# Kernel optimization log

Hardware: AMD Instinct MI355X
Metric: run time of the kernel (lower is better)

## Reference

```python
import jax, jax.numpy as jnp
import numpy as np

N = 8192
E = 262144
C = 256          # in_channels
OUT = 256        # out_channels
H = 4            # num_heads
DH = C // H      # head dim


def setup_inputs() -> dict:
    key = jax.random.key(0)
    ks = jax.random.split(key, 12)
    stdv = 1.0 / np.sqrt(C)
    inp = {
        "x": jax.random.normal(ks[0], (N, C), dtype=jnp.float32),
        "adj": jax.random.randint(ks[1], (2, E), 0, N, dtype=jnp.int64),
        "weight_local": jax.random.uniform(ks[2], (C, C), jnp.float32, -stdv, stdv),
        # nn.MultiheadAttention packed projections
        "in_proj_w": jax.random.normal(ks[3], (3 * C, C), jnp.float32) * stdv,
        "in_proj_b": jnp.zeros((3 * C,), jnp.float32),
        "out_proj_w": jax.random.normal(ks[4], (C, C), jnp.float32) * stdv,
        "out_proj_b": jnp.zeros((C,), jnp.float32),
        "ln_g": jnp.ones((C,), jnp.float32),
        "ln_b": jnp.zeros((C,), jnp.float32),
        "alpha": jnp.zeros((), jnp.float32),
        "fc_w": jax.random.normal(ks[5], (OUT, C), jnp.float32) * stdv,
        "fc_b": jnp.zeros((OUT,), jnp.float32),
    }
    return inp


def _gcn_conv(x, edge_index):
    # out[col] += (1/sqrt(d[col]*d[row])) * x[row], d = in-degree by col
    row, col = edge_index[0], edge_index[1]
    n = x.shape[0]
    d = jax.ops.segment_sum(jnp.ones((edge_index.shape[1],), x.dtype), col, num_segments=n)
    val = jax.lax.rsqrt(d[col] * d[row])
    val = jnp.where(jnp.isfinite(val), val, 0.0)
    msg = x[row] * val[:, None]                      # [E, C] gather + scale
    return jax.ops.segment_sum(msg, col, num_segments=n)  # [N, C] scatter-add


def _mha(x, in_proj_w, in_proj_b, out_proj_w, out_proj_b):
    # single-batch self-attention over all N nodes
    qkv = x @ in_proj_w.T + in_proj_b                # [N, 3C]
    q, k, v = jnp.split(qkv, 3, axis=-1)
    def heads(t):
        return t.reshape(N, H, DH).transpose(1, 0, 2)  # [H, N, DH]
    q, k, v = heads(q), heads(k), heads(v)
    scores = jnp.einsum("hnd,hmd->hnm", q, k) / np.sqrt(DH)  # [H, N, N]
    attn = jax.nn.softmax(scores, axis=-1)
    out = jnp.einsum("hnm,hmd->hnd", attn, v)        # [H, N, DH]
    out = out.transpose(1, 0, 2).reshape(N, C)
    return out @ out_proj_w.T + out_proj_b


def _layernorm(x, g, b, eps=1e-5):
    mu = jnp.mean(x, axis=-1, keepdims=True)
    var = jnp.var(x, axis=-1, keepdims=True)
    return (x - mu) * jax.lax.rsqrt(var + eps) * g + b


def reference(x, adj, weight_local, in_proj_w, in_proj_b, out_proj_w, out_proj_b,
              ln_g, ln_b, alpha, fc_w, fc_b):
    hi = _gcn_conv(x, adj)
    local_embed = hi @ weight_local                   # [N, C]
    attn_out = _mha(x, in_proj_w, in_proj_b, out_proj_w, out_proj_b)
    global_embed = _layernorm(x + attn_out, ln_g, ln_b)
    w = jax.nn.sigmoid(alpha)
    combined = w * local_embed + (1.0 - w) * global_embed
    return combined @ fc_w.T + fc_b                   # [N, OUT]
```

## Files before the change

### kernel.cpp

```cpp
#include <hip/hip_runtime.h>
#include <hip/hip_bf16.h>
#include <math.h>

#define NN   8192
#define EE   262144
#define CC   256
#define HH   4

typedef __bf16 bf16;
typedef __bf16 bf16x8 __attribute__((ext_vector_type(8)));
typedef __bf16 bf16x4 __attribute__((ext_vector_type(4)));
typedef __bf16 bf16x2 __attribute__((ext_vector_type(2)));
typedef float  f32x4  __attribute__((ext_vector_type(4)));

static __device__ __forceinline__ bf16 f2bf(float f) { return (bf16)f; }

static __device__ __forceinline__ unsigned pk2(float a, float b) {
    __hip_bfloat162 h = __float22bfloat162_rn(float2{a, b});
    return *reinterpret_cast<unsigned*>(&h);
}

__global__ void prep_all(const float* __restrict__ x, bf16* __restrict__ xb,
                         const float* __restrict__ ipw, const float* __restrict__ opw,
                         const float* __restrict__ fcw, const float* __restrict__ wloc,
                         bf16* __restrict__ ipwb, bf16* __restrict__ opwb,
                         bf16* __restrict__ fcwb, bf16* __restrict__ wlTb,
                         const int* __restrict__ adj, int* __restrict__ ideg) {
    int b = blockIdx.x, t = threadIdx.x;
    if (b < 2048) {
        for (int i = b * 256 + t; i < NN * CC; i += 2048 * 256) xb[i] = f2bf(x[i]);
    } else if (b < 2816) { int i = (b - 2048) * 256 + t; ipwb[i] = f2bf(ipw[i]); }
    else if (b < 3072)   { int i = (b - 2816) * 256 + t; opwb[i] = f2bf(opw[i]); }
    else if (b < 3328)   { int i = (b - 3072) * 256 + t; fcwb[i] = f2bf(fcw[i]); }
    else if (b < 3584)   { int n = b - 3328;             wlTb[n * 256 + t] = f2bf(wloc[t * 256 + n]); }
    else {
        int e = (b - 3584) * 256 + t;
        if (e < EE) atomicAdd(&ideg[adj[EE + e]], 1);
    }
}

__global__ __launch_bounds__(256) void build_kv(const bf16* __restrict__ qkv,
                                                bf16* __restrict__ Kpk,
                                                bf16* __restrict__ Vpk) {
    __shared__ bf16 tl[64][72];
    const int bx = blockIdx.x;
    const int h  = blockIdx.y;
    const int tid = threadIdx.x;
    #pragma unroll
    for (int i = 0; i < 2; i++) {
        int u = tid + i * 256;
        int key = u >> 3, g = u & 7;
        *reinterpret_cast<bf16x8*>(&tl[key][g * 8]) =
            *reinterpret_cast<const bf16x8*>(qkv + (size_t)(bx * 64 + key) * 768 + 256 + h * 64 + g * 8);
    }
    __syncthreads();
    #pragma unroll
    for (int i = 0; i < 2; i++) {
        int ee = tid + i * 256;
        int l15 = ee & 15, quad = (ee >> 4) & 3, c = (ee >> 6) & 1, ktl = ee >> 7;
        int key_local = (ktl >> 1) * 32 + (l15 >> 2) * 8 + (ktl & 1) * 4 + (l15 & 3);
        bf16x8 v = *reinterpret_cast<const bf16x8*>(&tl[key_local][c * 32 + quad * 8]);
        *reinterpret_cast<bf16x8*>(Kpk + ((size_t)((h * 512 + bx * 4 + ktl) * 2 + c)) * 512
                                       + (quad * 16 + l15) * 8) = v;
    }
    __syncthreads();
    #pragma unroll
    for (int i = 0; i < 2; i++) {
        int u = tid + i * 256;
        int key = u >> 3, g = u & 7;
        *reinterpret_cast<bf16x8*>(&tl[key][g * 8]) =
            *reinterpret_cast<const bf16x8*>(qkv + (size_t)(bx * 64 + key) * 768 + 512 + h * 64 + g * 8);
    }
    __syncthreads();
    #pragma unroll
    for (int i = 0; i < 2; i++) {
        int ee = tid + i * 256;
        int l15 = ee & 15, quad = (ee >> 4) & 3, nt = (ee >> 6) & 3, kcl = ee >> 8;
        bf16x8 v;
        #pragma unroll
        for (int j = 0; j < 8; j++) v[j] = tl[kcl * 32 + quad * 8 + j][nt * 16 + l15];
        *reinterpret_cast<bf16x8*>(Vpk + ((size_t)((h * 256 + bx * 2 + kcl) * 4 + nt)) * 512
                                       + (quad * 16 + l15) * 8) = v;
    }
}

__global__ __launch_bounds__(256) void scan_offsets(const int* __restrict__ ideg,
        int* __restrict__ off, int* __restrict__ cursor, float* __restrict__ rs) {
    __shared__ int ps[256];
    const int tid = threadIdx.x;
    const int base = tid * 32;
    int loc[32];
    int s = 0;
    #pragma unroll
    for (int i = 0; i < 32; i++) { loc[i] = s; s += ideg[base + i]; }
    ps[tid] = s;
    __syncthreads();
    for (int d = 1; d < 256; d <<= 1) {
        int v = (tid >= d) ? ps[tid - d] : 0;
        __syncthreads();
        ps[tid] += v;
        __syncthreads();
    }
    int excl = ps[tid] - s;
    #pragma unroll
    for (int i = 0; i < 32; i++) {
        int o = excl + loc[i];
        off[base + i] = o;
        cursor[base + i] = o;
        int dg = ideg[base + i];
        rs[base + i] = dg > 0 ? rsqrtf((float)dg) : 0.f;
    }
    if (tid == 255) off[8192] = excl + s;
}

__global__ void fill_csr(const int* __restrict__ adj, int* __restrict__ cursor,
                         int* __restrict__ csr) {
    int e = blockIdx.x * 256 + threadIdx.x;
    if (e < EE) {
        int col = adj[EE + e];
        int pos = atomicAdd(&cursor[col], 1);
        csr[pos] = adj[e];
    }
}

__global__ __launch_bounds__(256) void gcn_gather3(const bf16* __restrict__ xb,
        const int* __restrict__ csr, const int* __restrict__ off,
        const float* __restrict__ rs, bf16* __restrict__ hib) {
    const int node = blockIdx.x * 2 + (threadIdx.x >> 7);
    const int j = threadIdx.x & 127;
    const int o = off[node];
    const int cnt = off[node + 1] - o;
    const float rsc = rs[node];
    const unsigned* xrow = (const unsigned*)xb;
    float a0 = 0.f, a1 = 0.f;
    int e = 0;
    for (; e + 8 <= cnt; e += 8) {
        int r[8];
        float v[8];
        unsigned u[8];
        #pragma unroll
        for (int i = 0; i < 8; i++) r[i] = csr[o + e + i];
        #pragma unroll
        for (int i = 0; i < 8; i++) v[i] = rsc * rs[r[i]];
        #pragma unroll
        for (int i = 0; i < 8; i++) u[i] = xrow[(size_t)r[i] * 128 + j];
        #pragma unroll
        for (int i = 0; i < 8; i++) {
            a0 += __uint_as_float(u[i] << 16) * v[i];
            a1 += __uint_as_float(u[i] & 0xffff0000u) * v[i];
        }
    }
    for (; e < cnt; e++) {
        int r0 = csr[o + e];
        float v0 = rsc * rs[r0];
        unsigned u0 = xrow[(size_t)r0 * 128 + j];
        a0 += __uint_as_float(u0 << 16) * v0;
        a1 += __uint_as_float(u0 & 0xffff0000u) * v0;
    }
    bf16x2 pk;
    pk[0] = f2bf(a0);
    pk[1] = f2bf(a1);
    ((bf16x2*)(hib + (size_t)node * CC))[j] = pk;
}

__global__ __launch_bounds__(256) void gemm_bt(
        const bf16* __restrict__ A, const bf16* __restrict__ W,
        const float* __restrict__ bias,
        float* __restrict__ outF, bf16* __restrict__ outB,
        int M, int N, int K) {
    const int tid  = threadIdx.x;
    const int wave = tid >> 6;
    const int lane = tid & 63;
    const int quad = lane >> 4;
    const int l15  = lane & 15;
    const int m0 = blockIdx.x * 128;
    const int n0 = blockIdx.y * 64;

    __shared__ bf16 Alds[128][72];
    __shared__ bf16 Wlds[64][72];

    f32x4 acc[2][4];
    #pragma unroll
    for (int mt = 0; mt < 2; mt++)
        #pragma unroll
        for (int nt = 0; nt < 4; nt++)
            acc[mt][nt] = (f32x4){0.f, 0.f, 0.f, 0.f};

    for (int k0 = 0; k0 < K; k0 += 64) {
        #pragma unroll
        for (int i = 0; i < 4; i++) {
            int u = tid + i * 256;
            int r = u >> 3;
            int cp = u & 7;
            *reinterpret_cast<bf16x8*>(&Alds[r][cp * 8]) =
                *reinterpret_cast<const bf16x8*>(A + (size_t)(m0 + r) * K + k0 + cp * 8);
        }
        #pragma unroll
        for (int i = 0; i < 2; i++) {
            int u = tid + i * 256;
            int r = u >> 3;
            int cp = u & 7;
            *reinterpret_cast<bf16x8*>(&Wlds[r][cp * 8]) =
                *reinterpret_cast<const bf16x8*>(W + (size_t)(n0 + r) * K + k0 + cp * 8);
        }
        __syncthreads();
        #pragma unroll
        for (int c = 0; c < 2; c++) {
            bf16x8 af[2], wf[4];
            #pragma unroll
            for (int mt = 0; mt < 2; mt++)
                af[mt] = *reinterpret_cast<const bf16x8*>(&Alds[wave * 32 + mt * 16 + l15][c * 32 + quad * 8]);
            #pragma unroll
            for (int nt = 0; nt < 4; nt++)
                wf[nt] = *reinterpret_cast<const bf16x8*>(&Wlds[nt * 16 + l15][c * 32 + quad * 8]);
            #pragma unroll
            for (int mt = 0; mt < 2; mt++)
                #pragma unroll
                for (int nt = 0; nt < 4; nt++)
                    acc[mt][nt] = __builtin_amdgcn_mfma_f32_16x16x32_bf16(af[mt], wf[nt], acc[mt][nt], 0, 0, 0);
        }
        __syncthreads();
    }
    #pragma unroll
    for (int mt = 0; mt < 2; mt++)
        #pragma unroll
        for (int nt = 0; nt < 4; nt++)
            #pragma unroll
            for (int r = 0; r < 4; r++) {
                int m = m0 + wave * 32 + mt * 16 + quad * 4 + r;
                int n = n0 + nt * 16 + l15;
                float v = acc[mt][nt][r];
                if (bias) v += bias[n];
                if (outF) outF[(size_t)m * N + n] = v;
                else      outB[(size_t)m * N + n] = f2bf(v);
            }
}

__global__ __launch_bounds__(512, 2) void flash_attn10(const bf16* __restrict__ qkv,
                                                       const bf16* __restrict__ Kpk,
                                                       const bf16* __restrict__ Vpk,
                                                       bf16* __restrict__ attnO) {
    const int tid  = threadIdx.x;
    const int w    = tid >> 6;
    const int g    = w >> 2;
    const int k4   = w & 3;
    const int lane = tid & 63;
    const int quad = lane >> 4;
    const int l15  = lane & 15;
    const int bx = blockIdx.x;
    const int h  = bx & 3;
    const int qb = bx >> 2;
    const int qbase = qb * 128 + g * 64;

    __shared__ bf16 Osh[8][64][68];
    __shared__ float lsh[8][64];

    const float qs = 0.180336880f;
    bf16x8 qf[4][2];
    #pragma unroll
    for (int qt = 0; qt < 4; qt++)
        #pragma unroll
        for (int c = 0; c < 2; c++) {
            bf16x8 raw = *reinterpret_cast<const bf16x8*>(
                qkv + (size_t)(qbase + qt * 16 + l15) * 768 + h * 64 + c * 32 + quad * 8);
            #pragma unroll
            for (int j = 0; j < 8; j++) qf[qt][c][j] = f2bf((float)raw[j] * qs);
        }

    const bf16* Kb = Kpk + (size_t)h * 524288 + lane * 8;
    const bf16* Vb = Vpk + (size_t)h * 524288 + lane * 8;

    f32x4 oacc[4][4];
    #pragma unroll
    for (int qt = 0; qt < 4; qt++)
        #pragma unroll
        for (int nt = 0; nt < 4; nt++) oacc[qt][nt] = (f32x4){0.f, 0.f, 0.f, 0.f};
    f32x4 lacc[4];
    #pragma unroll
    for (int qt = 0; qt < 4; qt++) lacc[qt] = (f32x4){0.f, 0.f, 0.f, 0.f};
    bf16x8 onesf;
    #pragma unroll
    for (int j = 0; j < 8; j++) onesf[j] = f2bf(1.0f);
    const f32x4 z4 = (f32x4){0.f, 0.f, 0.f, 0.f};

    bf16x8 kfA[2][2], vfA[4], kfB[2][2], vfB[4];

    #define LOADKV(kc, kf, vf)                                                          \
        {                                                                               \
            _Pragma("unroll")                                                           \
            for (int s = 0; s < 2; s++)                                                 \
                _Pragma("unroll")                                                       \
                for (int c = 0; c < 2; c++)                                             \
                    kf[s][c] = *reinterpret_cast<const bf16x8*>(Kb + (kc) * 2048 + s * 1024 + c * 512); \
            _Pragma("unroll")                                                           \
            for (int nt = 0; nt < 4; nt++)                                              \
                vf[nt] = *reinterpret_cast<const bf16x8*>(Vb + (kc) * 2048 + nt * 512); \
        }

    #define COMPUTE(kf, vf)                                                             \
        {                                                                               \
            f32x4 sacc[2][4];                                                           \
            _Pragma("unroll")                                                           \
            for (int s = 0; s < 2; s++)                                                 \
                _Pragma("unroll")                                                       \
                for (int qt = 0; qt < 4; qt++) {                                        \
                    sacc[s][qt] = __builtin_amdgcn_mfma_f32_16x16x32_bf16(kf[s][0], qf[qt][0], z4, 0, 0, 0); \
                    sacc[s][qt] = __builtin_amdgcn_mfma_f32_16x16x32_bf16(kf[s][1], qf[qt][1], sacc[s][qt], 0, 0, 0); \
                }                                                                       \
            _Pragma("unroll")                                                           \
            for (int qt = 0; qt < 4; qt++) {                                            \
                float e0 = __builtin_amdgcn_exp2f(sacc[0][qt][0]);                      \
                float e1 = __builtin_amdgcn_exp2f(sacc[0][qt][1]);                      \
                float e2 = __builtin_amdgcn_exp2f(sacc[0][qt][2]);                      \
                float e3 = __builtin_amdgcn_exp2f(sacc[0][qt][3]);                      \
                float e4 = __builtin_amdgcn_exp2f(sacc[1][qt][0]);                      \
                float e5 = __builtin_amdgcn_exp2f(sacc[1][qt][1]);                      \
                float e6 = __builtin_amdgcn_exp2f(sacc[1][qt][2]);                      \
                float e7 = __builtin_amdgcn_exp2f(sacc[1][qt][3]);                      \
                union { bf16x8 v; unsigned u[4]; } pu;                                  \
                pu.u[0] = pk2(e0, e1);                                                  \
                pu.u[1] = pk2(e2, e3);                                                  \
                pu.u[2] = pk2(e4, e5);                                                  \
                pu.u[3] = pk2(e6, e7);                                                  \
                _Pragma("unroll")                                                       \
                for (int nt = 0; nt < 4; nt++)                                          \
                    oacc[qt][nt] = __builtin_amdgcn_mfma_f32_16x16x32_bf16(pu.v, vf[nt], oacc[qt][nt], 0, 0, 0); \
                lacc[qt] = __builtin_amdgcn_mfma_f32_16x16x32_bf16(pu.v, onesf, lacc[qt], 0, 0, 0); \
            }                                                                           \
        }

    LOADKV(k4, kfA, vfA);
    for (int it = 0; it < 64; it += 2) {
        const int kB = k4 + (it + 1) * 4;
        LOADKV(kB, kfB, vfB);
        COMPUTE(kfA, vfA);
        int kA2 = k4 + (it + 2) * 4;
        if (kA2 > 255) kA2 = k4;
        LOADKV(kA2, kfA, vfA);
        COMPUTE(kfB, vfB);
    }
    #undef LOADKV
    #undef COMPUTE

    #pragma unroll
    for (int qt = 0; qt < 4; qt++)
        #pragma unroll
        for (int nt = 0; nt < 4; nt++)
            #pragma unroll
            for (int r = 0; r < 4; r++)
                Osh[w][qt * 16 + quad * 4 + r][nt * 16 + l15] = f2bf(oacc[qt][nt][r]);
    if (l15 == 0) {
        #pragma unroll
        for (int qt = 0; qt < 4; qt++)
            #pragma unroll
            for (int r = 0; r < 4; r++)
                lsh[w][qt * 16 + quad * 4 + r] = lacc[qt][r];
    }
    __syncthreads();

    const int q7 = tid >> 2;
    const int gg = q7 >> 6;
    const int ql = q7 & 63;
    const int ds = (tid & 3) * 16;
    const int wb = gg * 4;
    float lsum = lsh[wb][ql] + lsh[wb + 1][ql] + lsh[wb + 2][ql] + lsh[wb + 3][ql];
    float linv = 1.f / lsum;
    float acc[16];
    #pragma unroll
    for (int i = 0; i < 16; i++) acc[i] = 0.f;
    #pragma unroll
    for (int v = 0; v < 4; v++) {
        bf16x8 o0 = *reinterpret_cast<const bf16x8*>(&Osh[wb + v][ql][ds]);
        bf16x8 o1 = *reinterpret_cast<const bf16x8*>(&Osh[wb + v][ql][ds + 8]);
        #pragma unroll
        for (int i = 0; i < 8; i++) { acc[i] += (float)o0[i]; acc[8 + i] += (float)o1[i]; }
    }
    bf16x8 ob0, ob1;
    #pragma unroll
    for (int i = 0; i < 8; i++) {
        ob0[i] = f2bf(acc[i] * linv);
        ob1[i] = f2bf(acc[8 + i] * linv);
    }
    bf16* dst = attnO + (size_t)(qb * 128 + q7) * CC + h * 64 + ds;
    *reinterpret_cast<bf16x8*>(dst) = ob0;
    *reinterpret_cast<bf16x8*>(dst + 8) = ob1;
}

__global__ __launch_bounds__(256) void gemm_ln_fc(
        const bf16* __restrict__ aOb, const bf16* __restrict__ opwb, const float* __restrict__ opb,
        const bf16* __restrict__ hib, const bf16* __restrict__ wlTb,
        const float* __restrict__ x, const float* __restrict__ lng, const float* __restrict__ lnb,
        const float* __restrict__ alp, const bf16* __restrict__ fcwb, const float* __restrict__ fcb,
        float* __restrict__ out) {
    const int tid = threadIdx.x;
    const int w = tid >> 6, lane = tid & 63, quad = lane >> 4, l15 = lane & 15;
    const int m0 = blockIdx.x * 16;
    const int n0w = w * 64;
    const f32x4 z4 = (f32x4){0.f, 0.f, 0.f, 0.f};

    __shared__ bf16 Ab[16][264];
    __shared__ float Xl[16][260];
    __shared__ float rsum[4][16], rsq[4][16];

    #pragma unroll
    for (int i = 0; i < 4; i++) {
        int u = tid + i * 256;
        int row = u >> 6, cp = (u & 63) * 4;
        *reinterpret_cast<f32x4*>(&Xl[row][cp]) =
            *reinterpret_cast<const f32x4*>(x + (size_t)(m0 + row) * CC + cp);
    }

    #pragma unroll
    for (int i = 0; i < 2; i++) {
        int u = tid + i * 256;
        int row = u >> 5, cp = (u & 31) * 8;
        *reinterpret_cast<bf16x8*>(&Ab[row][cp]) =
            *reinterpret_cast<const bf16x8*>(aOb + (size_t)(m0 + row) * CC + cp);
    }
    __syncthreads();
    f32x4 r0[4], r1[4], acc[4];
    #pragma unroll
    for (int nt = 0; nt < 4; nt++) acc[nt] = z4;
    for (int kc = 0; kc < 4; kc++)
        #pragma unroll
        for (int c = 0; c < 2; c++) {
            bf16x8 af = *reinterpret_cast<const bf16x8*>(&Ab[l15][kc * 64 + c * 32 + quad * 8]);
            #pragma unroll
            for (int nt = 0; nt < 4; nt++) {
                bf16x8 wf = *reinterpret_cast<const bf16x8*>(
                    opwb + (size_t)(n0w + nt * 16 + l15) * CC + kc * 64 + c * 32 + quad * 8);
                acc[nt] = __builtin_amdgcn_mfma_f32_16x16x32_bf16(af, wf, acc[nt], 0, 0, 0);
            }
        }
    #pragma unroll
    for (int nt = 0; nt < 4; nt++) r0[nt] = acc[nt];
    __syncthreads();

    #pragma unroll
    for (int i = 0; i < 2; i++) {
        int u = tid + i * 256;
        int row = u >> 5, cp = (u & 31) * 8;
        *reinterpret_cast<bf16x8*>(&Ab[row][cp]) =
            *reinterpret_cast<const bf16x8*>(hib + (size_t)(m0 + row) * CC + cp);
    }
    __syncthreads();
    #pragma unroll
    for (int nt = 0; nt < 4; nt++) acc[nt] = z4;
    for (int kc = 0; kc < 4; kc++)
        #pragma unroll
        for (int c = 0; c < 2; c++) {
            bf16x8 af = *reinterpret_cast<const bf16x8*>(&Ab[l15][kc * 64 + c * 32 + quad * 8]);
            #pragma unroll
            for (int nt = 0; nt < 4; nt++) {
                bf16x8 wf = *reinterpret_cast<const bf16x8*>(
                    wlTb + (size_t)(n0w + nt * 16 + l15) * CC + kc * 64 + c * 32 + quad * 8);
                acc[nt] = __builtin_amdgcn_mfma_f32_16x16x32_bf16(af, wf, acc[nt], 0, 0, 0);
            }
        }
    #pragma unroll
    for (int nt = 0; nt < 4; nt++) r1[nt] = acc[nt];
    __syncthreads();

    float v[4][4];
    #pragma unroll
    for (int nt = 0; nt < 4; nt++) {
        float bias0 = opb[n0w + nt * 16 + l15];
        #pragma unroll
        for (int r = 0; r < 4; r++)
            v[nt][r] = Xl[quad * 4 + r][n0w + nt * 16 + l15] + r0[nt][r] + bias0;
    }
    #pragma unroll
    for (int r = 0; r < 4; r++) {
        float s = v[0][r] + v[1][r] + v[2][r] + v[3][r];
        float s2 = v[0][r] * v[0][r] + v[1][r] * v[1][r] + v[2][r] * v[2][r] + v[3][r] * v[3][r];
        #pragma unroll
        for (int o = 1; o < 16; o <<= 1) { s += __shfl_xor(s, o); s2 += __shfl_xor(s2, o); }
        if (l15 == 0) { rsum[w][quad * 4 + r] = s; rsq[w][quad * 4 + r] = s2; }
    }
    __syncthreads();

    const float wgt = 1.f / (1.f + __expf(-alp[0]));
    float gv[4], bv[4], fb[4];
    #pragma unroll
    for (int nt = 0; nt < 4; nt++) {
        int n = n0w + nt * 16 + l15;
        gv[nt] = lng[n]; bv[nt] = lnb[n]; fb[nt] = fcb[n];
    }
    #pragma unroll
    for (int r = 0; r < 4; r++) {
        int row = quad * 4 + r;
        float S = rsum[0][row] + rsum[1][row] + rsum[2][row] + rsum[3][row];
        float S2 = rsq[0][row] + rsq[1][row] + rsq[2][row] + rsq[3][row];
        float mu = S * (1.f / CC);
        float var = S2 * (1.f / CC) - mu * mu;
        float rstd = rsqrtf(var + 1e-5f);
        #pragma unroll
        for (int nt = 0; nt < 4; nt++) {
            float ln = (v[nt][r] - mu) * rstd * gv[nt] + bv[nt];
            float cmb = wgt * r1[nt][r] + (1.f - wgt) * ln;
            Ab[row][n0w + nt * 16 + l15] = f2bf(cmb);
        }
    }
    __syncthreads();

    #pragma unroll
    for (int nt = 0; nt < 4; nt++) acc[nt] = z4;
    for (int kc = 0; kc < 4; kc++)
        #pragma unroll
        for (int c = 0; c < 2; c++) {
            bf16x8 af = *reinterpret_cast<const bf16x8*>(&Ab[l15][kc * 64 + c * 32 + quad * 8]);
            #pragma unroll
            for (int nt = 0; nt < 4; nt++) {
                bf16x8 wf = *reinterpret_cast<const bf16x8*>(
                    fcwb + (size_t)(n0w + nt * 16 + l15) * CC + kc * 64 + c * 32 + quad * 8);
                acc[nt] = __builtin_amdgcn_mfma_f32_16x16x32_bf16(af, wf, acc[nt], 0, 0, 0);
            }
        }
    #pragma unroll
    for (int nt = 0; nt < 4; nt++)
        #pragma unroll
        for (int r = 0; r < 4; r++)
            out[(size_t)(m0 + quad * 4 + r) * CC + n0w + nt * 16 + l15] = acc[nt][r] + fb[nt];
}

extern "C" void kernel_launch(void* const* d_in, const int* in_sizes, int n_in,
                              void* d_out, int out_size, void* d_ws, size_t ws_size,
                              hipStream_t stream) {
    (void)in_sizes; (void)n_in; (void)out_size; (void)ws_size;
    const float* x    = (const float*)d_in[0];
    const int*   adj  = (const int*)d_in[1];
    const float* wloc = (const float*)d_in[2];
    const float* ipw  = (const float*)d_in[3];
    const float* ipb  = (const float*)d_in[4];
    const float* opw  = (const float*)d_in[5];
    const float* opb  = (const float*)d_in[6];
    const float* lng  = (const float*)d_in[7];
    const float* lnb  = (const float*)d_in[8];
    const float* alp  = (const float*)d_in[9];
    const float* fcw  = (const float*)d_in[10];
    const float* fcb  = (const float*)d_in[11];
    float* out = (float*)d_out;

    char* p = (char*)d_ws;
    int*   ideg   = (int*)p;    p += (size_t)NN * 4;
    int*   off    = (int*)p;    p += (size_t)(NN + 1) * 4;
    int*   cursor = (int*)p;    p += (size_t)NN * 4;
    float* rs     = (float*)p;  p += (size_t)NN * 4;
    int*   csr    = (int*)p;    p += (size_t)EE * 4;
    bf16* xb    = (bf16*)p;   p += (size_t)NN * CC * 2;
    bf16* hib   = (bf16*)p;   p += (size_t)NN * CC * 2;
    bf16* ipwb  = (bf16*)p;   p += (size_t)768 * 256 * 2;
    bf16* wlTb  = (bf16*)p;   p += (size_t)256 * 256 * 2;
    bf16* opwb  = (bf16*)p;   p += (size_t)256 * 256 * 2;
    bf16* fcwb  = (bf16*)p;   p += (size_t)256 * 256 * 2;
    bf16* qkvb  = (bf16*)p;   p += (size_t)NN * 768 * 2;
    bf16* Kpk   = (bf16*)p;   p += (size_t)HH * 512 * 2 * 512 * 2;
    bf16* Vpk   = (bf16*)p;   p += (size_t)HH * 256 * 4 * 512 * 2;
    bf16* aOb   = (bf16*)p;   p += (size_t)NN * CC * 2;

    hipMemsetAsync(ideg, 0, (size_t)NN * 4, stream);

    prep_all<<<4608, 256, 0, stream>>>(x, xb, ipw, opw, fcw, wloc, ipwb, opwb, fcwb, wlTb, adj, ideg);
    scan_offsets<<<1, 256, 0, stream>>>(ideg, off, cursor, rs);
    fill_csr<<<EE / 256, 256, 0, stream>>>(adj, cursor, csr);
    gcn_gather3<<<NN / 2, 256, 0, stream>>>(xb, csr, off, rs, hib);

    gemm_bt<<<dim3(NN / 128, 768 / 64), 256, 0, stream>>>(xb, ipwb, ipb, nullptr, qkvb, NN, 768, 256);
    build_kv<<<dim3(NN / 64, HH), 256, 0, stream>>>(qkvb, Kpk, Vpk);
    flash_attn10<<<256, 512, 0, stream>>>(qkvb, Kpk, Vpk, aOb);
    gemm_ln_fc<<<NN / 16, 256, 0, stream>>>(aOb, opwb, opb, hib, wlTb, x, lng, lnb, alp, fcwb, fcb, out);
}
```

Measured before the change: 249.4 us.

## Stage shared K/V tiles in LDS via async global-to-LDS loads in flash attention

The attention kernel now has both 4-wave groups of a block share one K/V tile. That tile is double-buffered in shared memory and filled with global_load_lds, replacing per-wave direct register loads from global memory. The query tile per wave group drops from 64 to 32 rows, so the grid doubles to 512 blocks and the occupancy hint rises to 4. The O/l reduction buffers reuse the K/V shared memory. This aims to halve global K/V traffic per block and improve latency hiding, at the cost of a block-wide barrier every iteration and fewer queries reusing each loaded K/V fragment.

```diff
diff --git a/kernel.cpp b/kernel.cpp
--- a/kernel.cpp
+++ b/kernel.cpp
@@ -18,6 +18,11 @@
 static __device__ __forceinline__ unsigned pk2(float a, float b) {
     __hip_bfloat162 h = __float22bfloat162_rn(float2{a, b});
     return *reinterpret_cast<unsigned*>(&h);
+}
+
+static __device__ __forceinline__ void gload_lds16(const bf16* g, bf16* l) {
+    __builtin_amdgcn_global_load_lds((const __attribute__((address_space(1))) void*)g,
+                                     (__attribute__((address_space(3))) void*)l, 16, 0, 0);
 }
 
 __global__ void prep_all(const float* __restrict__ x, bf16* __restrict__ xb,
@@ -236,7 +241,7 @@
             }
 }
 
-__global__ __launch_bounds__(512, 2) void flash_attn10(const bf16* __restrict__ qkv,
+__global__ __launch_bounds__(512, 4) void flash_attn11(const bf16* __restrict__ qkv,
                                                        const bf16* __restrict__ Kpk,
                                                        const bf16* __restrict__ Vpk,
                                                        bf16* __restrict__ attnO) {
@@ -250,65 +255,69 @@
     const int bx = blockIdx.x;
     const int h  = bx & 3;
     const int qb = bx >> 2;
-    const int qbase = qb * 128 + g * 64;
-
-    __shared__ bf16 Osh[8][64][68];
-    __shared__ float lsh[8][64];
+    const int qbase = qb * 64;
+
+    __shared__ bf16 KV[2][16384];
 
     const float qs = 0.180336880f;
-    bf16x8 qf[4][2];
-    #pragma unroll
-    for (int qt = 0; qt < 4; qt++)
+    bf16x8 qf[2][2];
+    #pragma unroll
+    for (int qt = 0; qt < 2; qt++)
         #pragma unroll
         for (int c = 0; c < 2; c++) {
             bf16x8 raw = *reinterpret_cast<const bf16x8*>(
-                qkv + (size_t)(qbase + qt * 16 + l15) * 768 + h * 64 + c * 32 + quad * 8);
+                qkv + (size_t)(qbase + g * 32 + qt * 16 + l15) * 768 + h * 64 + c * 32 + quad * 8);
             #pragma unroll
             for (int j = 0; j < 8; j++) qf[qt][c][j] = f2bf((float)raw[j] * qs);
         }
 
-    const bf16* Kb = Kpk + (size_t)h * 524288 + lane * 8;
-    const bf16* Vb = Vpk + (size_t)h * 524288 + lane * 8;
-
-    f32x4 oacc[4][4];
-    #pragma unroll
-    for (int qt = 0; qt < 4; qt++)
+    f32x4 oacc[2][4];
+    #pragma unroll
+    for (int qt = 0; qt < 2; qt++)
         #pragma unroll
         for (int nt = 0; nt < 4; nt++) oacc[qt][nt] = (f32x4){0.f, 0.f, 0.f, 0.f};
-    f32x4 lacc[4];
-    #pragma unroll
-    for (int qt = 0; qt < 4; qt++) lacc[qt] = (f32x4){0.f, 0.f, 0.f, 0.f};
+    f32x4 lacc[2];
+    #pragma unroll
+    for (int qt = 0; qt < 2; qt++) lacc[qt] = (f32x4){0.f, 0.f, 0.f, 0.f};
     bf16x8 onesf;
     #pragma unroll
     for (int j = 0; j < 8; j++) onesf[j] = f2bf(1.0f);
     const f32x4 z4 = (f32x4){0.f, 0.f, 0.f, 0.f};
 
-    bf16x8 kfA[2][2], vfA[4], kfB[2][2], vfB[4];
-
-    #define LOADKV(kc, kf, vf)                                                          \
+    const bf16* ssrc = (g == 0 ? Kpk : Vpk) + (size_t)h * 524288 + (size_t)lane * 8;
+    const int dbase = (g ? 8192 : 0) + k4 * 2048;
+
+    #define STAGE(buf, step)                                                            \
         {                                                                               \
+            size_t sb = (size_t)((step) * 4 + k4) * 2048;                               \
+            _Pragma("unroll")                                                           \
+            for (int i = 0; i < 4; i++)                                                 \
+                gload_lds16(ssrc + sb + i * 512, &KV[buf][dbase + i * 512]);            \
+        }
+
+    #define COMPUTE(buf)                                                                \
+        {                                                                               \
+            bf16x8 kf[2][2], vf[4];                                                     \
             _Pragma("unroll")                                                           \
             for (int s = 0; s < 2; s++)                                                 \
                 _Pragma("unroll")                                                       \
                 for (int c = 0; c < 2; c++)                                             \
-                    kf[s][c] = *reinterpret_cast<const bf16x8*>(Kb + (kc) * 2048 + s * 1024 + c * 512); \
+                    kf[s][c] = *reinterpret_cast<const bf16x8*>(                        \
+                        &KV[buf][k4 * 2048 + s * 1024 + c * 512 + lane * 8]);           \
             _Pragma("unroll")                                                           \
             for (int nt = 0; nt < 4; nt++)                                              \
-                vf[nt] = *reinterpret_cast<const bf16x8*>(Vb + (kc) * 2048 + nt * 512); \
-        }
-
-    #define COMPUTE(kf, vf)                                                             \
-        {                                                                               \
-            f32x4 sacc[2][4];                                                           \
+                vf[nt] = *reinterpret_cast<const bf16x8*>(                              \
+                    &KV[buf][8192 + k4 * 2048 + nt * 512 + lane * 8]);                  \
+            f32x4 sacc[2][2];                                                           \
             _Pragma("unroll")                                                           \
             for (int s = 0; s < 2; s++)                                                 \
                 _Pragma("unroll")                                                       \
-                for (int qt = 0; qt < 4; qt++) {                                        \
+                for (int qt = 0; qt < 2; qt++) {                                        \
                     sacc[s][qt] = __builtin_amdgcn_mfma_f32_16x16x32_bf16(kf[s][0], qf[qt][0], z4, 0, 0, 0); \
                     sacc[s][qt] = __builtin_amdgcn_mfma_f32_16x16x32_bf16(kf[s][1], qf[qt][1], sacc[s][qt], 0, 0, 0); \
                 }                                                                       \
             _Pragma("unroll")                                                           \
-            for (int qt = 0; qt < 4; qt++) {                                            \
+            for (int qt = 0; qt < 2; qt++) {                                            \
                 float e0 = __builtin_amdgcn_exp2f(sacc[0][qt][0]);                      \
                 float e1 = __builtin_amdgcn_exp2f(sacc[0][qt][1]);                      \
                 float e2 = __builtin_amdgcn_exp2f(sacc[0][qt][2]);                      \
@@ -329,21 +338,22 @@
             }                                                                           \
         }
 
-    LOADKV(k4, kfA, vfA);
-    for (int it = 0; it < 64; it += 2) {
-        const int kB = k4 + (it + 1) * 4;
-        LOADKV(kB, kfB, vfB);
-        COMPUTE(kfA, vfA);
-        int kA2 = k4 + (it + 2) * 4;
-        if (kA2 > 255) kA2 = k4;
-        LOADKV(kA2, kfA, vfA);
-        COMPUTE(kfB, vfB);
-    }
-    #undef LOADKV
+    STAGE(0, 0);
+    __syncthreads();
+    for (int it = 0; it < 64; ++it) {
+        const int cur = it & 1;
+        if (it < 63) STAGE(cur ^ 1, it + 1);
+        COMPUTE(cur);
+        __syncthreads();
+    }
+    #undef STAGE
     #undef COMPUTE
 
-    #pragma unroll
-    for (int qt = 0; qt < 4; qt++)
+    bf16 (*Osh)[32][68] = reinterpret_cast<bf16 (*)[32][68]>(&KV[0][0]);
+    float* lshp = reinterpret_cast<float*>(reinterpret_cast<char*>(&KV[0][0]) + 34816);
+
+    #pragma unroll
+    for (int qt = 0; qt < 2; qt++)
         #pragma unroll
         for (int nt = 0; nt < 4; nt++)
             #pragma unroll
@@ -351,39 +361,34 @@
                 Osh[w][qt * 16 + quad * 4 + r][nt * 16 + l15] = f2bf(oacc[qt][nt][r]);
     if (l15 == 0) {
         #pragma unroll
-        for (int qt = 0; qt < 4; qt++)
+        for (int qt = 0; qt < 2; qt++)
             #pragma unroll
             for (int r = 0; r < 4; r++)
-                lsh[w][qt * 16 + quad * 4 + r] = lacc[qt][r];
-    }
-    __syncthreads();
-
-    const int q7 = tid >> 2;
-    const int gg = q7 >> 6;
-    const int ql = q7 & 63;
-    const int ds = (tid & 3) * 16;
-    const int wb = gg * 4;
-    float lsum = lsh[wb][ql] + lsh[wb + 1][ql] + lsh[wb + 2][ql] + lsh[wb + 3][ql];
+                lshp[w * 32 + qt * 16 + quad * 4 + r] = lacc[qt][r];
+    }
+    __syncthreads();
+
+    const int q6 = tid >> 3;
+    const int ds = (tid & 7) * 8;
+    const int gq = q6 >> 5;
+    const int ql = q6 & 31;
+    const int wb = gq * 4;
+    float lsum = lshp[wb * 32 + ql] + lshp[(wb + 1) * 32 + ql]
+               + lshp[(wb + 2) * 32 + ql] + lshp[(wb + 3) * 32 + ql];
     float linv = 1.f / lsum;
-    float acc[16];
-    #pragma unroll
-    for (int i = 0; i < 16; i++) acc[i] = 0.f;
+    float acc[8];
+    #pragma unroll
+    for (int i = 0; i < 8; i++) acc[i] = 0.f;
     #pragma unroll
     for (int v = 0; v < 4; v++) {
-        bf16x8 o0 = *reinterpret_cast<const bf16x8*>(&Osh[wb + v][ql][ds]);
-        bf16x8 o1 = *reinterpret_cast<const bf16x8*>(&Osh[wb + v][ql][ds + 8]);
-        #pragma unroll
-        for (int i = 0; i < 8; i++) { acc[i] += (float)o0[i]; acc[8 + i] += (float)o1[i]; }
-    }
-    bf16x8 ob0, ob1;
-    #pragma unroll
-    for (int i = 0; i < 8; i++) {
-        ob0[i] = f2bf(acc[i] * linv);
-        ob1[i] = f2bf(acc[8 + i] * linv);
-    }
-    bf16* dst = attnO + (size_t)(qb * 128 + q7) * CC + h * 64 + ds;
-    *reinterpret_cast<bf16x8*>(dst) = ob0;
-    *reinterpret_cast<bf16x8*>(dst + 8) = ob1;
+        bf16x8 o = *reinterpret_cast<const bf16x8*>(&Osh[wb + v][ql][ds]);
+        #pragma unroll
+        for (int i = 0; i < 8; i++) acc[i] += (float)o[i];
+    }
+    bf16x8 ob;
+    #pragma unroll
+    for (int i = 0; i < 8; i++) ob[i] = f2bf(acc[i] * linv);
+    *reinterpret_cast<bf16x8*>(attnO + (size_t)(qbase + q6) * CC + h * 64 + ds) = ob;
 }
 
 __global__ __launch_bounds__(256) void gemm_ln_fc(
@@ -567,6 +572,6 @@
 
     gemm_bt<<<dim3(NN / 128, 768 / 64), 256, 0, stream>>>(xb, ipwb, ipb, nullptr, qkvb, NN, 768, 256);
     build_kv<<<dim3(NN / 64, HH), 256, 0, stream>>>(qkvb, Kpk, Vpk);
-    flash_attn10<<<256, 512, 0, stream>>>(qkvb, Kpk, Vpk, aOb);
+    flash_attn11<<<512, 512, 0, stream>>>(qkvb, Kpk, Vpk, aOb);
     gemm_ln_fc<<<NN / 16, 256, 0, stream>>>(aOb, opwb, opb, hib, wlTb, x, lng, lnb, alp, fcwb, fcb, out);
 }
```

New measurement: 267.6 us. +7.3%, slower.

## Split attention keys across two blocks and combine partial sums in a new kernel

Applied to the files above, without the earlier changes.

Splits the flash-attention key range in half, so 512 blocks each process half the keys. Each block writes unnormalized fp32 partial outputs and row sums, and a new combine kernel adds the two halves and normalizes. The goal is to fill more CUs, since 256 blocks underfilled the GPU. The change also raises the launch-bounds occupancy hint and adds s_setprio around the MFMA sections. In exchange it pays for an extra kernel launch and the round trip of the fp32 partials through memory.

```diff
diff --git a/kernel.cpp b/kernel.cpp
--- a/kernel.cpp
+++ b/kernel.cpp
@@ -236,10 +236,11 @@
             }
 }
 
-__global__ __launch_bounds__(512, 2) void flash_attn10(const bf16* __restrict__ qkv,
+__global__ __launch_bounds__(512, 4) void flash_attn14(const bf16* __restrict__ qkv,
                                                        const bf16* __restrict__ Kpk,
                                                        const bf16* __restrict__ Vpk,
-                                                       bf16* __restrict__ attnO) {
+                                                       float* __restrict__ Opf,
+                                                       float* __restrict__ lpf) {
     const int tid  = threadIdx.x;
     const int w    = tid >> 6;
     const int g    = w >> 2;
@@ -249,8 +250,10 @@
     const int l15  = lane & 15;
     const int bx = blockIdx.x;
     const int h  = bx & 3;
-    const int qb = bx >> 2;
+    const int qb = (bx >> 2) & 63;
+    const int kh = bx >> 8;
     const int qbase = qb * 128 + g * 64;
+    const int cb = kh * 128;
 
     __shared__ bf16 Osh[8][64][68];
     __shared__ float lsh[8][64];
@@ -291,15 +294,16 @@
             for (int s = 0; s < 2; s++)                                                 \
                 _Pragma("unroll")                                                       \
                 for (int c = 0; c < 2; c++)                                             \
-                    kf[s][c] = *reinterpret_cast<const bf16x8*>(Kb + (kc) * 2048 + s * 1024 + c * 512); \
+                    kf[s][c] = *reinterpret_cast<const bf16x8*>(Kb + (size_t)(kc) * 2048 + s * 1024 + c * 512); \
             _Pragma("unroll")                                                           \
             for (int nt = 0; nt < 4; nt++)                                              \
-                vf[nt] = *reinterpret_cast<const bf16x8*>(Vb + (kc) * 2048 + nt * 512); \
+                vf[nt] = *reinterpret_cast<const bf16x8*>(Vb + (size_t)(kc) * 2048 + nt * 512); \
         }
 
     #define COMPUTE(kf, vf)                                                             \
         {                                                                               \
             f32x4 sacc[2][4];                                                           \
+            __builtin_amdgcn_s_setprio(1);                                              \
             _Pragma("unroll")                                                           \
             for (int s = 0; s < 2; s++)                                                 \
                 _Pragma("unroll")                                                       \
@@ -307,6 +311,7 @@
                     sacc[s][qt] = __builtin_amdgcn_mfma_f32_16x16x32_bf16(kf[s][0], qf[qt][0], z4, 0, 0, 0); \
                     sacc[s][qt] = __builtin_amdgcn_mfma_f32_16x16x32_bf16(kf[s][1], qf[qt][1], sacc[s][qt], 0, 0, 0); \
                 }                                                                       \
+            __builtin_amdgcn_s_setprio(0);                                              \
             _Pragma("unroll")                                                           \
             for (int qt = 0; qt < 4; qt++) {                                            \
                 float e0 = __builtin_amdgcn_exp2f(sacc[0][qt][0]);                      \
@@ -322,20 +327,22 @@
                 pu.u[1] = pk2(e2, e3);                                                  \
                 pu.u[2] = pk2(e4, e5);                                                  \
                 pu.u[3] = pk2(e6, e7);                                                  \
+                __builtin_amdgcn_s_setprio(1);                                          \
                 _Pragma("unroll")                                                       \
                 for (int nt = 0; nt < 4; nt++)                                          \
                     oacc[qt][nt] = __builtin_amdgcn_mfma_f32_16x16x32_bf16(pu.v, vf[nt], oacc[qt][nt], 0, 0, 0); \
                 lacc[qt] = __builtin_amdgcn_mfma_f32_16x16x32_bf16(pu.v, onesf, lacc[qt], 0, 0, 0); \
+                __builtin_amdgcn_s_setprio(0);                                          \
             }                                                                           \
         }
 
-    LOADKV(k4, kfA, vfA);
-    for (int it = 0; it < 64; it += 2) {
-        const int kB = k4 + (it + 1) * 4;
+    LOADKV(cb + k4, kfA, vfA);
+    for (int it = 0; it < 32; it += 2) {
+        const int kB = cb + k4 + (it + 1) * 4;
         LOADKV(kB, kfB, vfB);
         COMPUTE(kfA, vfA);
-        int kA2 = k4 + (it + 2) * 4;
-        if (kA2 > 255) kA2 = k4;
+        int kA2 = cb + k4 + (it + 2) * 4;
+        if (it + 2 >= 32) kA2 = cb + k4;
         LOADKV(kA2, kfA, vfA);
         COMPUTE(kfB, vfB);
     }
@@ -364,7 +371,6 @@
     const int ds = (tid & 3) * 16;
     const int wb = gg * 4;
     float lsum = lsh[wb][ql] + lsh[wb + 1][ql] + lsh[wb + 2][ql] + lsh[wb + 3][ql];
-    float linv = 1.f / lsum;
     float acc[16];
     #pragma unroll
     for (int i = 0; i < 16; i++) acc[i] = 0.f;
@@ -375,15 +381,35 @@
         #pragma unroll
         for (int i = 0; i < 8; i++) { acc[i] += (float)o0[i]; acc[8 + i] += (float)o1[i]; }
     }
-    bf16x8 ob0, ob1;
-    #pragma unroll
-    for (int i = 0; i < 8; i++) {
-        ob0[i] = f2bf(acc[i] * linv);
-        ob1[i] = f2bf(acc[8 + i] * linv);
-    }
-    bf16* dst = attnO + (size_t)(qb * 128 + q7) * CC + h * 64 + ds;
-    *reinterpret_cast<bf16x8*>(dst) = ob0;
-    *reinterpret_cast<bf16x8*>(dst + 8) = ob1;
+    float* od = Opf + (size_t)bx * 8192 + q7 * 64 + ds;
+    #pragma unroll
+    for (int p4 = 0; p4 < 4; p4++) {
+        f32x4 v4 = (f32x4){acc[p4 * 4], acc[p4 * 4 + 1], acc[p4 * 4 + 2], acc[p4 * 4 + 3]};
+        *reinterpret_cast<f32x4*>(od + p4 * 4) = v4;
+    }
+    if ((tid & 3) == 0) lpf[bx * 128 + q7] = lsum;
+}
+
+__global__ __launch_bounds__(256) void combine_attn(const float* __restrict__ Opf,
+                                                    const float* __restrict__ lpf,
+                                                    bf16* __restrict__ attnO) {
+    const int gid = blockIdx.x * 256 + threadIdx.x;
+    const int d   = (gid & 15) * 4;
+    const int q7  = (gid >> 4) & 127;
+    const int rest = gid >> 11;
+    const int h  = rest & 3;
+    const int qb = rest >> 2;
+    const int sA = qb * 4 + h;
+    const int sB = sA + 256;
+    const float la = lpf[sA * 128 + q7];
+    const float lb = lpf[sB * 128 + q7];
+    const float linv = 1.f / (la + lb);
+    f32x4 oa = *reinterpret_cast<const f32x4*>(Opf + (size_t)sA * 8192 + q7 * 64 + d);
+    f32x4 ob = *reinterpret_cast<const f32x4*>(Opf + (size_t)sB * 8192 + q7 * 64 + d);
+    bf16x4 r;
+    #pragma unroll
+    for (int i = 0; i < 4; i++) r[i] = f2bf((oa[i] + ob[i]) * linv);
+    *reinterpret_cast<bf16x4*>(attnO + (size_t)(qb * 128 + q7) * CC + h * 64 + d) = r;
 }
 
 __global__ __launch_bounds__(256) void gemm_ln_fc(
@@ -557,6 +583,8 @@
     bf16* Kpk   = (bf16*)p;   p += (size_t)HH * 512 * 2 * 512 * 2;
     bf16* Vpk   = (bf16*)p;   p += (size_t)HH * 256 * 4 * 512 * 2;
     bf16* aOb   = (bf16*)p;   p += (size_t)NN * CC * 2;
+    float* Opf  = (float*)p;  p += (size_t)512 * 128 * 64 * 4;
+    float* lpf  = (float*)p;  p += (size_t)512 * 128 * 4;
 
     hipMemsetAsync(ideg, 0, (size_t)NN * 4, stream);
 
@@ -567,6 +595,7 @@
 
     gemm_bt<<<dim3(NN / 128, 768 / 64), 256, 0, stream>>>(xb, ipwb, ipb, nullptr, qkvb, NN, 768, 256);
     build_kv<<<dim3(NN / 64, HH), 256, 0, stream>>>(qkvb, Kpk, Vpk);
-    flash_attn10<<<256, 512, 0, stream>>>(qkvb, Kpk, Vpk, aOb);
+    flash_attn14<<<512, 512, 0, stream>>>(qkvb, Kpk, Vpk, Opf, lpf);
+    combine_attn<<<2048, 256, 0, stream>>>(Opf, lpf, aOb);
     gemm_ln_fc<<<NN / 16, 256, 0, stream>>>(aOb, opwb, opb, hib, wlTb, x, lng, lnb, alp, fcwb, fcb, out);
 }
```

Measured after the change: 940.1 us. +277.0%, slower.
